# Performance work log

Measured on AMD Instinct MI355X. Metric: run time of the kernel, lower is better.

The kernel has to match this reference:

```python
import jax, jax.numpy as jnp
import numpy as np

C = 128        # in_channels
HEADS = 4
B, D, H, W = 4, 16, 64, 64  # H must equal W for this module's matmul to type-check


def conv1x1(x, Wm, b):
    # 1x1x1 Conv3d == per-voxel linear over channels
    return jnp.einsum('bcdhw,oc->bodhw', x, Wm) + b[None, :, None, None, None]


def setup_inputs() -> dict:
    key = jax.random.key(0)
    ks = jax.random.split(key, 14)
    scale = 1.0 / np.sqrt(C)

    def wmat(k):
        return jax.random.normal(k, (C, C), jnp.float32) * scale

    def bvec(k):
        return jax.random.normal(k, (C,), jnp.float32) * 0.01

    return {
        'x':  jax.random.normal(ks[0], (B, C, D, H, W), jnp.float32),
        'Wq': wmat(ks[1]),  'bq': bvec(ks[2]),
        'Wk': wmat(ks[3]),  'bk': bvec(ks[4]),
        'Wv': wmat(ks[5]),  'bv': bvec(ks[6]),
        'Wa1': wmat(ks[7]), 'ba1': bvec(ks[8]),
        'Wa2': wmat(ks[9]), 'ba2': bvec(ks[10]),
        'Wf': wmat(ks[11]), 'bf': bvec(ks[12]),
    }


def reference(x, Wq, bq, Wk, bk, Wv, bv, Wa1, ba1, Wa2, ba2, Wf, bf):
    b, c, d, h, w = x.shape
    ch = c // HEADS  # channels per head

    q = conv1x1(x, Wq, bq).reshape(b, HEADS, ch, d, h, w)
    k = conv1x1(x, Wk, bk).reshape(b, HEADS, ch, d, h, w)
    v = conv1x1(x, Wv, bv).reshape(b, HEADS, ch, d, h, w)

    # attention over the last spatial axis: (W, H)^T @ (H, W) -> (W, W)
    attn = jnp.einsum('bhcdxi,bhcdxj->bhcdij', q, k)  # [b, heads, ch, d, W, W]
    attn = jax.nn.softmax(attn, axis=-1)
    # (W, W) @ (H=W, W) -> (W, W)
    out = jnp.einsum('bhcdik,bhcdkj->bhcdij', attn, v)
    out = out.reshape(b, c, d, h, w)

    # depth=1 attention layer: conv1x1 -> relu -> conv1x1
    out = conv1x1(jax.nn.relu(conv1x1(out, Wa1, ba1)), Wa2, ba2)
    out = conv1x1(out, Wf, bf)
    return out
```

## Files before the change

### kernel.cpp

```cpp
#include <hip/hip_runtime.h>


#define CCH 128
#define SPB 65536
#define NBATCH 4
#define WTAB 16384

typedef float f32x4 __attribute__((ext_vector_type(4)));
typedef __bf16 bf16x8 __attribute__((ext_vector_type(8)));
typedef short s16x8 __attribute__((ext_vector_type(8)));
typedef unsigned short u16x8 __attribute__((ext_vector_type(8)));
typedef unsigned short u16x4 __attribute__((ext_vector_type(4)));
typedef unsigned int u32x2 __attribute__((ext_vector_type(2)));

template <typename T>
static __device__ __forceinline__ auto mfma_try(T a, T b, f32x4 c, int)
    -> decltype(__builtin_amdgcn_mfma_f32_16x16x32_bf16(a, b, c, 0, 0, 0)) {
  return __builtin_amdgcn_mfma_f32_16x16x32_bf16(a, b, c, 0, 0, 0);
}
template <typename T>
static __device__ __forceinline__ f32x4 mfma_try(T a, T b, f32x4 c, long) {
  return __builtin_amdgcn_mfma_f32_16x16x32_bf16(
      __builtin_bit_cast(bf16x8, a), __builtin_bit_cast(bf16x8, b), c, 0, 0, 0);
}
static __device__ __forceinline__ f32x4 MFMA16(u16x8 a, u16x8 b, f32x4 c) {
  return mfma_try(__builtin_bit_cast(s16x8, a), __builtin_bit_cast(s16x8, b), c, 0);
}

static __device__ __forceinline__ unsigned short f2b(float f) {
  return __builtin_bit_cast(unsigned short, (__bf16)f);
}
static __device__ __forceinline__ unsigned int pk2(float a, float b) {
  return (unsigned int)f2b(a) | ((unsigned int)f2b(b) << 16);
}

static __device__ __forceinline__ void glds16(const unsigned short* g,
                                              unsigned short* l) {
  __builtin_amdgcn_global_load_lds(
      (const __attribute__((address_space(1))) unsigned int*)g,
      (__attribute__((address_space(3))) unsigned int*)l, 16, 0, 0);
}

static __device__ __forceinline__ void bar_lgkm() {
  asm volatile("s_waitcnt lgkmcnt(0)" ::: "memory");
  __builtin_amdgcn_sched_barrier(0);
  __builtin_amdgcn_s_barrier();
  __builtin_amdgcn_sched_barrier(0);
}
static __device__ __forceinline__ void bar_vm0() {
  asm volatile("s_waitcnt vmcnt(0)" ::: "memory");
  __builtin_amdgcn_sched_barrier(0);
  __builtin_amdgcn_s_barrier();
  __builtin_amdgcn_sched_barrier(0);
}
static __device__ __forceinline__ void bar_vm4_lgkm() {
  asm volatile("s_waitcnt vmcnt(4) lgkmcnt(0)" ::: "memory");
  __builtin_amdgcn_sched_barrier(0);
  __builtin_amdgcn_s_barrier();
  __builtin_amdgcn_sched_barrier(0);
}

static __device__ __forceinline__ int swzc(int r, int c) {
  int slot = ((c >> 3) ^ (r & 7) ^ ((r >> 3) & 15)) & 15;
  return r * 128 + slot * 8 + (c & 7);
}
static __device__ __forceinline__ int widx(int r, int c) {
  return (r & 64) * 128 + swzc(r & 63, c);
}
static __device__ __forceinline__ int cbix(int o, int s) {
  int slot = ((s >> 3) ^ (o & 15)) & 15;
  return o * 128 + slot * 8 + (s & 7);
}
static __device__ __forceinline__ int swat(int w, int x) {
  int slot = ((x >> 3) ^ (w & 7) ^ ((w >> 3) & 7)) & 7;
  return w * 64 + slot * 8 + (x & 7);
}
static __device__ __forceinline__ int pix(int i, int j) {
  int slot = ((j >> 3) ^ (((i >> 2) & 3) << 1)) & 7;
  return i * 64 + slot * 8 + (j & 7);
}

__global__ __launch_bounds__(256) void prep_w_kernel(
    const float* __restrict__ Wq, const float* __restrict__ Wk,
    const float* __restrict__ Wv, const float* __restrict__ W1,
    const float* __restrict__ W2, const float* __restrict__ W3,
    unsigned short* __restrict__ out)
{
  const float* Ws[6] = {Wq, Wk, Wv, W1, W2, W3};
  const float* W = Ws[blockIdx.x];
  unsigned short* o = out + (size_t)blockIdx.x * WTAB;
  const int tid = threadIdx.x;
#pragma unroll
  for (int p = 0; p < 16; ++p) {
    const int base = p * 1024 + tid * 4;
    const int m = base >> 7;
    const int c0 = base & 127;
    f32x4 v = *(const f32x4*)&W[base];
    u16x4 u;
#pragma unroll
    for (int e = 0; e < 4; ++e) u[e] = f2b(v[e]);
    *(u16x4*)&o[widx(m, c0)] = u;
  }
}

__global__ __launch_bounds__(512, 2) void qkv_kernel(
    const float* __restrict__ X, const unsigned short* __restrict__ Wbf,
    const float* __restrict__ Bq, const float* __restrict__ Bk,
    const float* __restrict__ Bv,
    unsigned short* __restrict__ Yq, unsigned short* __restrict__ Yk,
    unsigned short* __restrict__ Yv)
{
  __shared__ unsigned short wt[WTAB];
  __shared__ unsigned short xb[WTAB];
  __shared__ float bias_lds[3][128];

  const int tid  = threadIdx.x;
  const int wv   = tid >> 6;
  const int lane = tid & 63;
  const int lr   = lane & 15;
  const int lg   = lane >> 4;
  const int lin  = blockIdx.x;
  const int swz  = ((lin & 7) << 6) | (lin >> 3);
  const int sbase = (swz & 127) * 512;
  const size_t xoff = (size_t)(swz >> 7) * CCH * SPB;
  const int go = tid * 8;

#pragma unroll
  for (int p = 0; p < 4; ++p) glds16(&Wbf[p * 4096 + go], &wt[p * 4096 + go]);

  if (tid < 128) {
    bias_lds[0][tid] = Bq[tid];
    bias_lds[1][tid] = Bk[tid];
    bias_lds[2][tid] = Bv[tid];
  }

  const int c0  = (tid >> 3) * 2;
  const int sb8 = (tid & 7) * 4;
  const float* xrow = X + xoff + (size_t)c0 * SPB + sbase;
  unsigned int* xb32 = (unsigned int*)xb;

  f32x4 xr[8];
#pragma unroll
  for (int i = 0; i < 4; ++i) {
    xr[i]     = *(const f32x4*)&xrow[sb8 + 32 * i];
    xr[4 + i] = *(const f32x4*)&xrow[SPB + sb8 + 32 * i];
  }
#pragma unroll
  for (int i = 0; i < 4; ++i)
#pragma unroll
    for (int e = 0; e < 4; ++e)
      xb32[swzc(sb8 + 32 * i + e, c0) >> 1] = pk2(xr[i][e], xr[4 + i][e]);
  __syncthreads();

#pragma unroll
  for (int si = 0; si < 4; ++si) {
    const int sg = sbase + si * 128;

    u16x8 afr[4];
#pragma unroll
    for (int ks = 0; ks < 4; ++ks)
      afr[ks] = *(const u16x8*)&xb[swzc(wv * 16 + lr, ks * 32 + lg * 8)];

    if (si < 3) {
      const float* xn = xrow + (si + 1) * 128;
#pragma unroll
      for (int i = 0; i < 4; ++i) {
        xr[i]     = *(const f32x4*)&xn[sb8 + 32 * i];
        xr[4 + i] = *(const f32x4*)&xn[SPB + sb8 + 32 * i];
      }
    }
    bar_lgkm();

    auto conv = [&](int ci, const unsigned short* Wnext,
                    unsigned short* __restrict__ Y, bool last) {
      f32x4 acc[8];
#pragma unroll
      for (int of = 0; of < 8; ++of) {
        f32x4 z = {0.f, 0.f, 0.f, 0.f};
        acc[of] = z;
      }
#pragma unroll
      for (int ks = 0; ks < 4; ++ks) {
        const int k0 = ks * 32 + lg * 8;
#pragma unroll
        for (int of = 0; of < 8; ++of) {
          u16x8 wfr = *(const u16x8*)&wt[widx(of * 16 + lr, k0)];
          acc[of] = MFMA16(afr[ks], wfr, acc[of]);
        }
      }
      bar_lgkm();
      if (Wnext) {
#pragma unroll
        for (int p = 0; p < 4; ++p)
          glds16(&Wnext[p * 4096 + go], &wt[p * 4096 + go]);
      }
#pragma unroll
      for (int of = 0; of < 8; ++of) {
        const float b = bias_lds[ci][of * 16 + lr];
        u32x2 pk;
        pk.x = pk2(acc[of][0] + b, acc[of][1] + b);
        pk.y = pk2(acc[of][2] + b, acc[of][3] + b);
        *(u32x2*)&xb[cbix(of * 16 + lr, wv * 16 + lg * 4)] = pk;
      }
      bar_lgkm();
#pragma unroll
      for (int p = 0; p < 4; ++p) {
        const int row = p * 32 + (tid >> 4);
        const int sc  = (tid & 15) * 8;
        u16x8 v = *(const u16x8*)&xb[cbix(row, sc)];
        *(u16x8*)&Y[xoff + (size_t)row * SPB + sg + sc] = v;
      }
      if (!last) bar_vm4_lgkm();
    };

    conv(0, Wbf + WTAB,     Yq, false);
    conv(1, Wbf + 2 * WTAB, Yk, false);
    conv(2, si < 3 ? Wbf : nullptr, Yv, si == 3);

    if (si < 3) {
#pragma unroll
      for (int i = 0; i < 4; ++i)
#pragma unroll
        for (int e = 0; e < 4; ++e)
          xb32[swzc(sb8 + 32 * i + e, c0) >> 1] = pk2(xr[i][e], xr[4 + i][e]);
      bar_lgkm();
    }
  }
}

__global__ __launch_bounds__(256, 4) void attn64_kernel(
    const unsigned short* __restrict__ Q,
    const unsigned short* __restrict__ K,
    const unsigned short* __restrict__ V,
    unsigned short* __restrict__ O)
{
  __shared__ unsigned short qt[4096];
  __shared__ unsigned short kt[4096];
  __shared__ unsigned short vt[4096];
  __shared__ unsigned short pbuf[4096];

  const int tid  = threadIdx.x;
  const int wv   = tid >> 6;
  const int lane = tid & 63;
  const int lr   = lane & 15;
  const int lg   = lane >> 4;
  const int bid  = blockIdx.x;
  const int bs   = ((bid & 7) << 10) | (bid >> 3);
  const size_t base = (size_t)bs * 4096;

  {
    const int x0 = (tid >> 3) * 2;
    const int w0 = (tid & 7) * 8;
    const size_t ga = base + (size_t)x0 * 64 + w0;
    u16x8 qa = *(const u16x8*)&Q[ga], qb = *(const u16x8*)&Q[ga + 64];
    u16x8 ka = *(const u16x8*)&K[ga], kb = *(const u16x8*)&K[ga + 64];
    u16x8 va = *(const u16x8*)&V[ga], vb = *(const u16x8*)&V[ga + 64];
    unsigned int* qt32 = (unsigned int*)qt;
    unsigned int* kt32 = (unsigned int*)kt;
    unsigned int* vt32 = (unsigned int*)vt;
#pragma unroll
    for (int e = 0; e < 8; ++e) {
      const int idx = swat(w0 + e, x0) >> 1;
      qt32[idx] = (unsigned int)qa[e] | ((unsigned int)qb[e] << 16);
      kt32[idx] = (unsigned int)ka[e] | ((unsigned int)kb[e] << 16);
      vt32[idx] = (unsigned int)va[e] | ((unsigned int)vb[e] << 16);
    }
  }
  __syncthreads();

  f32x4 sacc[4];
#pragma unroll
  for (int nf = 0; nf < 4; ++nf) { f32x4 z = {0.f, 0.f, 0.f, 0.f}; sacc[nf] = z; }
#pragma unroll
  for (int ks = 0; ks < 2; ++ks) {
    const int k0 = ks * 32 + lg * 8;
    u16x8 a = *(const u16x8*)&qt[swat(wv * 16 + lr, k0)];
#pragma unroll
    for (int nf = 0; nf < 4; ++nf) {
      u16x8 bb = *(const u16x8*)&kt[swat(nf * 16 + lr, k0)];
      sacc[nf] = MFMA16(a, bb, sacc[nf]);
    }
  }

#pragma unroll
  for (int r = 0; r < 4; ++r) {
    float m = fmaxf(fmaxf(sacc[0][r], sacc[1][r]), fmaxf(sacc[2][r], sacc[3][r]));
    m = fmaxf(m, __shfl_xor(m, 1));
    m = fmaxf(m, __shfl_xor(m, 2));
    m = fmaxf(m, __shfl_xor(m, 4));
    m = fmaxf(m, __shfl_xor(m, 8));
    float sum = 0.f;
#pragma unroll
    for (int nf = 0; nf < 4; ++nf) {
      float p = __expf(sacc[nf][r] - m);
      sacc[nf][r] = p;
      sum += p;
    }
    sum += __shfl_xor(sum, 1);
    sum += __shfl_xor(sum, 2);
    sum += __shfl_xor(sum, 4);
    sum += __shfl_xor(sum, 8);
    const float inv = 1.f / sum;
    const int i = wv * 16 + lg * 4 + r;
#pragma unroll
    for (int nf = 0; nf < 4; ++nf)
      pbuf[pix(i, nf * 16 + lr)] = f2b(sacc[nf][r] * inv);
  }

  f32x4 oacc[4];
#pragma unroll
  for (int nf = 0; nf < 4; ++nf) { f32x4 z = {0.f, 0.f, 0.f, 0.f}; oacc[nf] = z; }
#pragma unroll
  for (int ks = 0; ks < 2; ++ks) {
    const int k0 = ks * 32 + lg * 8;
    u16x8 a = *(const u16x8*)&pbuf[pix(wv * 16 + lr, k0)];
#pragma unroll
    for (int nf = 0; nf < 4; ++nf) {
      u16x8 bb = *(const u16x8*)&vt[swat(nf * 16 + lr, k0)];
      oacc[nf] = MFMA16(bb, a, oacc[nf]);
    }
  }

  {
    const size_t ib = base + (size_t)(16 * wv + lr) * 64 + lg * 4;
#pragma unroll
    for (int nf = 0; nf < 4; ++nf) {
      u32x2 pk;
      pk.x = pk2(oacc[nf][0], oacc[nf][1]);
      pk.y = pk2(oacc[nf][2], oacc[nf][3]);
      *(u32x2*)&O[ib + nf * 16] = pk;
    }
  }
}

__global__ __launch_bounds__(256, 2) void tail_kernel(
    const unsigned short* __restrict__ Xb, const unsigned short* __restrict__ Wbf,
    const float* __restrict__ B1, const float* __restrict__ B2,
    const float* __restrict__ B3, float* __restrict__ OUT)
{
  __shared__ unsigned short wl[16384];
  __shared__ unsigned short xc[16384];
  __shared__ float bias_lds[3][128];

  const int tid  = threadIdx.x;
  const int wv   = tid >> 6;
  const int lane = tid & 63;
  const int lr   = lane & 15;
  const int lg   = lane >> 4;
  const int bx   = blockIdx.x;
  const int bxs  = ((bx & 7) << 6) | (bx >> 3);
  const int s0   = bxs * 128;
  const size_t xbase = (size_t)blockIdx.y * CCH * SPB;
  const int go = tid * 8;

#pragma unroll
  for (int p = 0; p < 8; ++p) glds16(&Wbf[p * 2048 + go], &wl[p * 2048 + go]);

  if (tid < 128) {
    bias_lds[0][tid] = B1[tid];
    bias_lds[1][tid] = B2[tid];
    bias_lds[2][tid] = B3[tid];
  }

  {
    const int cp = tid >> 2;
    const int sq = tid & 3;
    const unsigned short* xa = Xb + xbase + (size_t)(2 * cp) * SPB + s0 + sq * 32;
    const unsigned short* xb = xa + SPB;
    unsigned int* xc32 = (unsigned int*)xc;
#pragma unroll
    for (int i = 0; i < 4; ++i) {
      u16x8 a = *(const u16x8*)&xa[8 * i];
      u16x8 b = *(const u16x8*)&xb[8 * i];
#pragma unroll
      for (int e = 0; e < 8; ++e)
        xc32[swzc(sq * 32 + 8 * i + e, 2 * cp) >> 1] =
            (unsigned int)a[e] | ((unsigned int)b[e] << 16);
    }
  }
  __syncthreads();

  u16x8 bfr[2][4];
#pragma unroll
  for (int nf = 0; nf < 2; ++nf)
#pragma unroll
    for (int ks = 0; ks < 4; ++ks)
      bfr[nf][ks] = *(const u16x8*)&xc[swzc(wv * 32 + nf * 16 + lr, ks * 32 + lg * 8)];

  f32x4 acc[8][2];
  auto gemm_std = [&]() {
#pragma unroll
    for (int mf = 0; mf < 8; ++mf)
#pragma unroll
      for (int nf = 0; nf < 2; ++nf) {
        f32x4 z = {0.f, 0.f, 0.f, 0.f};
        acc[mf][nf] = z;
      }
#pragma unroll
    for (int ks = 0; ks < 4; ++ks) {
      const int k0 = ks * 32 + lg * 8;
#pragma unroll
      for (int mf = 0; mf < 8; ++mf) {
        u16x8 afr = *(const u16x8*)&wl[widx(mf * 16 + lr, k0)];
        acc[mf][0] = MFMA16(afr, bfr[0][ks], acc[mf][0]);
        acc[mf][1] = MFMA16(afr, bfr[1][ks], acc[mf][1]);
      }
    }
  };

  auto epi_chain = [&](int ci, bool relu) {
#pragma unroll
    for (int mf = 0; mf < 8; ++mf)
#pragma unroll
      for (int nf = 0; nf < 2; ++nf) {
        const int s = wv * 32 + nf * 16 + lr;
        const int cc = mf * 16 + lg * 4;
        f32x4 bb = *(const f32x4*)&bias_lds[ci][cc];
        float v0 = acc[mf][nf][0] + bb[0];
        float v1 = acc[mf][nf][1] + bb[1];
        float v2 = acc[mf][nf][2] + bb[2];
        float v3 = acc[mf][nf][3] + bb[3];
        if (relu) {
          v0 = fmaxf(v0, 0.f); v1 = fmaxf(v1, 0.f);
          v2 = fmaxf(v2, 0.f); v3 = fmaxf(v3, 0.f);
        }
        u32x2 pk;
        pk.x = pk2(v0, v1);
        pk.y = pk2(v2, v3);
        *(u32x2*)&xc[swzc(s, cc)] = pk;
      }
#pragma unroll
    for (int nf = 0; nf < 2; ++nf)
#pragma unroll
      for (int ks = 0; ks < 4; ++ks)
        bfr[nf][ks] = *(const u16x8*)&xc[swzc(wv * 32 + nf * 16 + lr, ks * 32 + lg * 8)];
  };

#pragma unroll
  for (int j = 0; j < 2; ++j) {
    gemm_std();
    bar_lgkm();
    const unsigned short* Wn = Wbf + (size_t)(j + 1) * WTAB;
#pragma unroll
    for (int p = 0; p < 8; ++p) glds16(&Wn[p * 2048 + go], &wl[p * 2048 + go]);
    epi_chain(j, j == 0);
    bar_vm0();
  }

  {
    f32x4 acc3[2][8];
#pragma unroll
    for (int sf = 0; sf < 2; ++sf)
#pragma unroll
      for (int of = 0; of < 8; ++of) {
        f32x4 z = {0.f, 0.f, 0.f, 0.f};
        acc3[sf][of] = z;
      }
#pragma unroll
    for (int ks = 0; ks < 4; ++ks) {
      const int k0 = ks * 32 + lg * 8;
#pragma unroll
      for (int of = 0; of < 8; ++of) {
        u16x8 wfr = *(const u16x8*)&wl[widx(of * 16 + lr, k0)];
        acc3[0][of] = MFMA16(bfr[0][ks], wfr, acc3[0][of]);
        acc3[1][of] = MFMA16(bfr[1][ks], wfr, acc3[1][of]);
      }
    }
    const int sb = s0 + wv * 32 + lg * 4;
#pragma unroll
    for (int sf = 0; sf < 2; ++sf)
#pragma unroll
      for (int of = 0; of < 8; ++of) {
        const float b = bias_lds[2][of * 16 + lr];
        f32x4 v = acc3[sf][of];
        v[0] += b; v[1] += b; v[2] += b; v[3] += b;
        *(f32x4*)&OUT[xbase + (size_t)(of * 16 + lr) * SPB + sb + sf * 16] = v;
      }
  }
}

extern "C" void kernel_launch(void* const* d_in, const int* in_sizes, int n_in,
                              void* d_out, int out_size, void* d_ws, size_t ws_size,
                              hipStream_t stream) {
  const float* x   = (const float*)d_in[0];
  const float* Wq  = (const float*)d_in[1];  const float* bq  = (const float*)d_in[2];
  const float* Wk  = (const float*)d_in[3];  const float* bk  = (const float*)d_in[4];
  const float* Wv  = (const float*)d_in[5];  const float* bv  = (const float*)d_in[6];
  const float* Wa1 = (const float*)d_in[7];  const float* ba1 = (const float*)d_in[8];
  const float* Wa2 = (const float*)d_in[9];  const float* ba2 = (const float*)d_in[10];
  const float* Wf  = (const float*)d_in[11]; const float* bf_ = (const float*)d_in[12];

  unsigned short* qb  = (unsigned short*)d_ws;
  unsigned short* wbf = qb + (size_t)NBATCH * CCH * SPB;
  unsigned short* kb = (unsigned short*)d_out;
  unsigned short* vb = kb + (size_t)NBATCH * CCH * SPB;

  prep_w_kernel<<<6, 256, 0, stream>>>(Wq, Wk, Wv, Wa1, Wa2, Wf, wbf);

  qkv_kernel<<<512, 512, 0, stream>>>(x, wbf, bq, bk, bv, qb, kb, vb);

  attn64_kernel<<<NBATCH * CCH * 16, 256, 0, stream>>>(qb, kb, vb, qb);

  tail_kernel<<<dim3(SPB / 128, NBATCH), 256, 0, stream>>>(
      qb, wbf + (size_t)3 * WTAB, ba1, ba2, bf_, (float*)d_out);
}
```

Baseline: 191.7 us.

## Keep all three QKV weight tiles resident in LDS and overlap conv stages

The QKV projection kernel now loads all three bf16 weight matrices into LDS once, instead of reloading one weight tile per conv stage with async global-to-LDS copies and vmcnt waits. Biases move from LDS into per-thread registers. The Q/K/V stages are software-pipelined so that the next projection's MFMAs run while the previous one's output is staged and stored, and V is written straight from registers in a strided pattern. LDS use rises from about 64KB to about 128KB per block, which may limit the declared two blocks per CU, and register pressure goes up.

After: 186.9 us. 2.5% less time.

```diff
diff --git a/kernel.cpp b/kernel.cpp
--- a/kernel.cpp
+++ b/kernel.cpp
@@ -49,12 +49,6 @@
 }
 static __device__ __forceinline__ void bar_vm0() {
   asm volatile("s_waitcnt vmcnt(0)" ::: "memory");
-  __builtin_amdgcn_sched_barrier(0);
-  __builtin_amdgcn_s_barrier();
-  __builtin_amdgcn_sched_barrier(0);
-}
-static __device__ __forceinline__ void bar_vm4_lgkm() {
-  asm volatile("s_waitcnt vmcnt(4) lgkmcnt(0)" ::: "memory");
   __builtin_amdgcn_sched_barrier(0);
   __builtin_amdgcn_s_barrier();
   __builtin_amdgcn_sched_barrier(0);
@@ -110,9 +104,8 @@
     unsigned short* __restrict__ Yq, unsigned short* __restrict__ Yk,
     unsigned short* __restrict__ Yv)
 {
-  __shared__ unsigned short wt[WTAB];
+  __shared__ unsigned short wt[3 * WTAB];
   __shared__ unsigned short xb[WTAB];
-  __shared__ float bias_lds[3][128];
 
   const int tid  = threadIdx.x;
   const int wv   = tid >> 6;
@@ -126,12 +119,17 @@
   const int go = tid * 8;
 
 #pragma unroll
-  for (int p = 0; p < 4; ++p) glds16(&Wbf[p * 4096 + go], &wt[p * 4096 + go]);
-
-  if (tid < 128) {
-    bias_lds[0][tid] = Bq[tid];
-    bias_lds[1][tid] = Bk[tid];
-    bias_lds[2][tid] = Bv[tid];
+  for (int t = 0; t < 3; ++t)
+#pragma unroll
+    for (int p = 0; p < 4; ++p)
+      glds16(&Wbf[t * WTAB + p * 4096 + go], &wt[t * WTAB + p * 4096 + go]);
+
+  float bq_v[8], bk_v[8], bv_v[8];
+#pragma unroll
+  for (int of = 0; of < 8; ++of) {
+    bq_v[of] = Bq[of * 16 + lr];
+    bk_v[of] = Bk[of * 16 + lr];
+    bv_v[of] = Bv[of * 16 + lr];
   }
 
   const int c0  = (tid >> 3) * 2;
@@ -156,11 +154,6 @@
   for (int si = 0; si < 4; ++si) {
     const int sg = sbase + si * 128;
 
-    u16x8 afr[4];
-#pragma unroll
-    for (int ks = 0; ks < 4; ++ks)
-      afr[ks] = *(const u16x8*)&xb[swzc(wv * 16 + lr, ks * 32 + lg * 8)];
-
     if (si < 3) {
       const float* xn = xrow + (si + 1) * 128;
 #pragma unroll
@@ -169,55 +162,92 @@
         xr[4 + i] = *(const f32x4*)&xn[SPB + sb8 + 32 * i];
       }
     }
+    u16x8 afr[4];
+#pragma unroll
+    for (int ks = 0; ks < 4; ++ks)
+      afr[ks] = *(const u16x8*)&xb[swzc(wv * 16 + lr, ks * 32 + lg * 8)];
     bar_lgkm();
 
-    auto conv = [&](int ci, const unsigned short* Wnext,
-                    unsigned short* __restrict__ Y, bool last) {
-      f32x4 acc[8];
+    f32x4 accq[8];
+#pragma unroll
+    for (int of = 0; of < 8; ++of) { f32x4 z = {0.f,0.f,0.f,0.f}; accq[of] = z; }
+#pragma unroll
+    for (int ks = 0; ks < 4; ++ks) {
+      const int k0 = ks * 32 + lg * 8;
+#pragma unroll
+      for (int of = 0; of < 8; ++of)
+        accq[of] = MFMA16(afr[ks], *(const u16x8*)&wt[widx(of*16+lr, k0)], accq[of]);
+    }
+#pragma unroll
+    for (int of = 0; of < 8; ++of) {
+      const float b = bq_v[of];
+      u32x2 pk;
+      pk.x = pk2(accq[of][0] + b, accq[of][1] + b);
+      pk.y = pk2(accq[of][2] + b, accq[of][3] + b);
+      *(u32x2*)&xb[cbix(of * 16 + lr, wv * 16 + lg * 4)] = pk;
+    }
+    bar_lgkm();
+
+    f32x4 acck[8];
+#pragma unroll
+    for (int of = 0; of < 8; ++of) { f32x4 z = {0.f,0.f,0.f,0.f}; acck[of] = z; }
+#pragma unroll
+    for (int ks = 0; ks < 4; ++ks) {
+      const int k0 = ks * 32 + lg * 8;
+#pragma unroll
+      for (int of = 0; of < 8; ++of)
+        acck[of] = MFMA16(afr[ks], *(const u16x8*)&wt[WTAB + widx(of*16+lr, k0)], acck[of]);
+    }
+#pragma unroll
+    for (int p = 0; p < 4; ++p) {
+      const int row = p * 32 + (tid >> 4);
+      const int sc  = (tid & 15) * 8;
+      u16x8 v = *(const u16x8*)&xb[cbix(row, sc)];
+      *(u16x8*)&Yq[xoff + (size_t)row * SPB + sg + sc] = v;
+    }
+    bar_lgkm();
+
+    f32x4 accv[8];
+#pragma unroll
+    for (int of = 0; of < 8; ++of) { f32x4 z = {0.f,0.f,0.f,0.f}; accv[of] = z; }
+#pragma unroll
+    for (int ks = 0; ks < 4; ++ks) {
+      const int k0 = ks * 32 + lg * 8;
+#pragma unroll
+      for (int of = 0; of < 8; ++of)
+        accv[of] = MFMA16(afr[ks], *(const u16x8*)&wt[2*WTAB + widx(of*16+lr, k0)], accv[of]);
+    }
+#pragma unroll
+    for (int of = 0; of < 8; ++of) {
+      const float b = bk_v[of];
+      u32x2 pk;
+      pk.x = pk2(acck[of][0] + b, acck[of][1] + b);
+      pk.y = pk2(acck[of][2] + b, acck[of][3] + b);
+      *(u32x2*)&xb[cbix(of * 16 + lr, wv * 16 + lg * 4)] = pk;
+    }
+    bar_lgkm();
+
+#pragma unroll
+    for (int p = 0; p < 4; ++p) {
+      const int row = p * 32 + (tid >> 4);
+      const int sc  = (tid & 15) * 8;
+      u16x8 v = *(const u16x8*)&xb[cbix(row, sc)];
+      *(u16x8*)&Yk[xoff + (size_t)row * SPB + sg + sc] = v;
+    }
+    {
+      const int sl = sg + wv * 16 + lg * 4;
 #pragma unroll
       for (int of = 0; of < 8; ++of) {
-        f32x4 z = {0.f, 0.f, 0.f, 0.f};
-        acc[of] = z;
-      }
-#pragma unroll
-      for (int ks = 0; ks < 4; ++ks) {
-        const int k0 = ks * 32 + lg * 8;
-#pragma unroll
-        for (int of = 0; of < 8; ++of) {
-          u16x8 wfr = *(const u16x8*)&wt[widx(of * 16 + lr, k0)];
-          acc[of] = MFMA16(afr[ks], wfr, acc[of]);
-        }
-      }
+        const float b = bv_v[of];
+        u32x2 pk;
+        pk.x = pk2(accv[of][0] + b, accv[of][1] + b);
+        pk.y = pk2(accv[of][2] + b, accv[of][3] + b);
+        *(u32x2*)&Yv[xoff + (size_t)(of * 16 + lr) * SPB + sl] = pk;
+      }
+    }
+
+    if (si < 3) {
       bar_lgkm();
-      if (Wnext) {
-#pragma unroll
-        for (int p = 0; p < 4; ++p)
-          glds16(&Wnext[p * 4096 + go], &wt[p * 4096 + go]);
-      }
-#pragma unroll
-      for (int of = 0; of < 8; ++of) {
-        const float b = bias_lds[ci][of * 16 + lr];
-        u32x2 pk;
-        pk.x = pk2(acc[of][0] + b, acc[of][1] + b);
-        pk.y = pk2(acc[of][2] + b, acc[of][3] + b);
-        *(u32x2*)&xb[cbix(of * 16 + lr, wv * 16 + lg * 4)] = pk;
-      }
-      bar_lgkm();
-#pragma unroll
-      for (int p = 0; p < 4; ++p) {
-        const int row = p * 32 + (tid >> 4);
-        const int sc  = (tid & 15) * 8;
-        u16x8 v = *(const u16x8*)&xb[cbix(row, sc)];
-        *(u16x8*)&Y[xoff + (size_t)row * SPB + sg + sc] = v;
-      }
-      if (!last) bar_vm4_lgkm();
-    };
-
-    conv(0, Wbf + WTAB,     Yq, false);
-    conv(1, Wbf + 2 * WTAB, Yk, false);
-    conv(2, si < 3 ? Wbf : nullptr, Yv, si == 3);
-
-    if (si < 3) {
 #pragma unroll
       for (int i = 0; i < 4; ++i)
 #pragma unroll
```
